# Optimization experiments

Measured on AMD Instinct MI355X. Metric: run time of the kernel, lower is better.

## Reference

```python
import jax, jax.numpy as jnp
import numpy as np

S, B, H = 4096, 1, 2048       # [seq, batch, hidden] layout (NeoX convention)
NP, HN = 16, H // 16          # heads, head dim
ROT = int(HN * 0.25)          # rotary_ndims = 32 (rotary_pct=0.25)
ROPE_BASE = 10000.0


def setup_inputs() -> dict:
    key = jax.random.key(0)
    k0, k1, k2 = jax.random.split(key, 3)
    hidden_states = jax.random.normal(k0, (S, B, H), jnp.float32) * 0.02
    # causal left-to-right mask: True = masked out (filled with -10000)
    attention_mask = jnp.triu(jnp.ones((1, 1, S, S), bool), k=1)
    w_qkv = jax.random.normal(k1, (3 * H, H), jnp.float32) * (1.0 / np.sqrt(H))
    w_dense = jax.random.normal(k2, (H, H), jnp.float32) * (1.0 / np.sqrt(H))
    b_dense = jnp.zeros((H,), jnp.float32)
    return {"hidden_states": hidden_states, "attention_mask": attention_mask,
            "w_qkv": w_qkv, "w_dense": w_dense, "b_dense": b_dense}


def _apply_rope(x, pos):
    # x: [s, b, np, ROT]; NeoX rotate_half convention
    inv_freq = 1.0 / (ROPE_BASE ** (jnp.arange(0, ROT, 2, dtype=jnp.float32) / ROT))
    freqs = pos[:, None] * inv_freq[None, :]              # [s, ROT/2]
    emb = jnp.concatenate([freqs, freqs], axis=-1)        # [s, ROT]
    cos = jnp.cos(emb)[:, None, None, :]
    sin = jnp.sin(emb)[:, None, None, :]
    x1, x2 = jnp.split(x, 2, axis=-1)
    rot = jnp.concatenate([-x2, x1], axis=-1)
    return x * cos + rot * sin


def reference(hidden_states, attention_mask, w_qkv, w_dense, b_dense):
    s, b, h = hidden_states.shape
    # fused QKV projection (no bias), reshape to [s, b, np, 3*hn], split
    qkv = (hidden_states @ w_qkv.T).reshape(s, b, NP, 3 * HN)
    q, k, v = jnp.split(qkv, 3, axis=-1)                  # each [s, b, np, hn]
    # partial rotary embedding on first ROT dims
    pos = jnp.arange(s, dtype=jnp.float32)
    q = jnp.concatenate([_apply_rope(q[..., :ROT], pos), q[..., ROT:]], axis=-1)
    k = jnp.concatenate([_apply_rope(k[..., :ROT], pos), k[..., ROT:]], axis=-1)
    # raw attention scores [b, np, s_q, s_k], scale 1/sqrt(hn)
    scores = jnp.einsum('sbhd,tbhd->bhst', q, k) / np.float32(np.sqrt(HN))
    # ltor mask: fill masked positions with -10000, softmax in fp32
    scores = jnp.where(attention_mask, jnp.float32(-10000.0), scores)
    probs = jax.nn.softmax(scores.astype(jnp.float32), axis=-1).astype(hidden_states.dtype)
    # context [s, b, np, hn] -> [s, b, h]
    ctx = jnp.einsum('bhst,tbhd->sbhd', probs, v).reshape(s, b, h)
    return ctx @ w_dense.T + b_dense
```

## Files before the change

### kernel.cpp

```cpp
#include <hip/hip_runtime.h>

#define S_LEN 4096
#define HID   2048
#define NHEAD 16
#define HDIM  128
#define QSCALE_L2E 0.12751664352f

typedef float  f32x4  __attribute__((ext_vector_type(4)));
typedef float  f32x16 __attribute__((ext_vector_type(16)));
typedef __bf16 bf16x8 __attribute__((ext_vector_type(8)));
typedef unsigned u32x4 __attribute__((ext_vector_type(4)));
typedef unsigned u32x2 __attribute__((ext_vector_type(2)));

#define MFMA16(a, b, c) __builtin_amdgcn_mfma_f32_16x16x32_bf16((a), (b), (c), 0, 0, 0)
#define MFMA32(a, b, c) __builtin_amdgcn_mfma_f32_32x32x16_bf16((a), (b), (c), 0, 0, 0)

__device__ __forceinline__ void gld16(const void* g, void* l) {
  __builtin_amdgcn_global_load_lds(
      (const __attribute__((address_space(1))) void*)(unsigned long long)(g),
      (__attribute__((address_space(3))) void*)(unsigned long long)(l),
      16, 0, 0);
}

__device__ __forceinline__ unsigned short f2bf(float f) {
  union { float f; unsigned u; } v; v.f = f;
  unsigned r = v.u + 0x7FFFu + ((v.u >> 16) & 1u);
  return (unsigned short)(r >> 16);
}
__device__ __forceinline__ float bf2f(unsigned short h) {
  union { unsigned u; float f; } v; v.u = ((unsigned)h) << 16;
  return v.f;
}
__device__ __forceinline__ unsigned cvtpk_bf16(float a, float b) {
  unsigned r;
  asm("v_cvt_pk_bf16_f32 %0, %1, %2" : "=v"(r) : "v"(a), "v"(b));
  return r;
}
__device__ __forceinline__ u32x2 pls(unsigned a, unsigned b) {
  return __builtin_amdgcn_permlane32_swap(a, b, false, false);
}
__device__ __forceinline__ float asf(unsigned u) { return __builtin_bit_cast(float, u); }
__device__ __forceinline__ unsigned asu(float f) { return __builtin_bit_cast(unsigned, f); }

__global__ __launch_bounds__(256) void cvt3_kernel(
    const float* __restrict__ s0, const float* __restrict__ s1,
    const float* __restrict__ s2, unsigned short* __restrict__ d0,
    unsigned short* __restrict__ d1, unsigned short* __restrict__ d2) {
  int i = (blockIdx.x * 256 + threadIdx.x) * 4;
  const float* src; unsigned short* dst;
  if (i < 8388608) { src = s0; dst = d0; }
  else if (i < 20971520) { src = s1 - 8388608; dst = d1 - 8388608; }
  else { src = s2 - 20971520; dst = d2 - 20971520; }
  const float4 v = *(const float4*)(src + i);
  ushort4 o;
  o.x = f2bf(v.x); o.y = f2bf(v.y); o.z = f2bf(v.z); o.w = f2bf(v.w);
  *(ushort4*)(dst + i) = o;
}

template <int EPI>
__global__ __launch_bounds__(512, 2) void gemm256_kernel(
    const unsigned short* __restrict__ A, const unsigned short* __restrict__ B,
    unsigned short* __restrict__ Qb, unsigned short* __restrict__ Kb,
    unsigned short* __restrict__ Vt,
    const float* __restrict__ bias, float* __restrict__ out) {
  __shared__ __align__(16) unsigned char sm[147456];
  constexpr int K = HID;
  constexpr int NT = K / 64;
  const int b = (int)blockIdx.x;
  const int bm = (b & 7) * 2 + ((b >> 3) & 1);
  const int bn = b >> 4;
  const int row0 = bm * 256, col0 = bn * 128;
  const int tid = threadIdx.x;
  const int wid = tid >> 6, lane = tid & 63;
  const int g = lane >> 4, r16 = lane & 15;
  const int wm = wid >> 1, wn = wid & 1;

  auto stageA = [&](int t, int bufo) {
    const int k0 = t * 64;
#pragma unroll
    for (int h = 0; h < 2; ++h)
#pragma unroll
      for (int cc = 0; cc < 2; ++cc) {
        const int chunk = cc * 512 + tid;
        const int r = chunk >> 3, c7 = chunk & 7;
        gld16(A + (row0 + h * 128 + r) * K + k0 + ((c7 ^ (r & 7)) << 3),
              sm + bufo + h * 16384 + chunk * 16);
      }
  };
  auto stageB = [&](int t, int bufo) {
    const int k0 = t * 64;
#pragma unroll
    for (int cc = 0; cc < 2; ++cc) {
      const int chunk = cc * 512 + tid;
      const int r = chunk >> 3, c7 = chunk & 7;
      gld16(B + (col0 + r) * K + k0 + ((c7 ^ (r & 7)) << 3),
            sm + bufo + 32768 + chunk * 16);
    }
  };

  f32x4 acc[4][4] = {};

  int aoff[4], boff[4];
#pragma unroll
  for (int m = 0; m < 4; ++m) {
    const int r = (wm & 1) * 64 + m * 16 + r16;
    aoff[m] = (wm >> 1) * 16384 + r * 128 + ((g * 16) ^ ((r & 7) << 4));
  }
#pragma unroll
  for (int n = 0; n < 4; ++n) {
    const int r = wn * 64 + n * 16 + r16;
    boff[n] = 32768 + r * 128 + ((g * 16) ^ ((r & 7) << 4));
  }

  stageA(0, 0); stageB(0, 0);
  stageA(1, 49152); stageB(1, 49152);
  asm volatile("s_waitcnt vmcnt(6)" ::: "memory");
  __builtin_amdgcn_s_barrier();
  __builtin_amdgcn_sched_barrier(0);

  int curo = 0, stgo = 98304;
  for (int t = 0; t < NT; ++t) {
    const bool st = (t + 2 < NT);
    bf16x8 af[4], bfv[4];
#pragma unroll
    for (int m = 0; m < 4; ++m) af[m] = *(const bf16x8*)(sm + curo + aoff[m]);
#pragma unroll
    for (int n = 0; n < 4; ++n) bfv[n] = *(const bf16x8*)(sm + curo + boff[n]);
    if (st) stageA(t + 2, stgo);
    __builtin_amdgcn_s_setprio(1);
#pragma unroll
    for (int m = 0; m < 4; ++m)
#pragma unroll
      for (int n = 0; n < 4; ++n) acc[m][n] = MFMA16(af[m], bfv[n], acc[m][n]);
    __builtin_amdgcn_s_setprio(0);
#pragma unroll
    for (int m = 0; m < 4; ++m) af[m] = *(const bf16x8*)(sm + curo + (aoff[m] ^ 64));
#pragma unroll
    for (int n = 0; n < 4; ++n) bfv[n] = *(const bf16x8*)(sm + curo + (boff[n] ^ 64));
    if (st) stageB(t + 2, stgo);
    __builtin_amdgcn_s_setprio(1);
#pragma unroll
    for (int m = 0; m < 4; ++m)
#pragma unroll
      for (int n = 0; n < 4; ++n) acc[m][n] = MFMA16(af[m], bfv[n], acc[m][n]);
    __builtin_amdgcn_s_setprio(0);
    if (st) asm volatile("s_waitcnt vmcnt(6)" ::: "memory");
    else    asm volatile("s_waitcnt vmcnt(0)" ::: "memory");
    __builtin_amdgcn_s_barrier();
    __builtin_amdgcn_sched_barrier(0);
    curo = (curo == 98304) ? 0 : curo + 49152;
    stgo = (stgo == 98304) ? 0 : stgo + 49152;
  }

  if constexpr (EPI == 0) {
    const int type = bn % 3, p = bn / 3;
    if (type <= 1) {
      unsigned short* Ob = (type == 0) ? Qb : Kb;
      const float qs = (type == 0) ? QSCALE_L2E : 1.0f;
      const float invf = exp2f(-(float)r16 * 0.8304820237218406f);
#pragma unroll
      for (int m = 0; m < 4; ++m) {
        const int s0 = row0 + wm * 64 + m * 16 + g * 4;
        if (wn == 0) {
#pragma unroll
          for (int r = 0; r < 4; ++r) {
            const float ang = (float)(s0 + r) * invf;
            const float c = cosf(ang), sn = sinf(ang);
            const float x = acc[m][0][r] * qs, y = acc[m][1][r] * qs;
            unsigned short* dst = Ob + (p * S_LEN + s0 + r) * HDIM;
            dst[r16]      = f2bf(x * c - y * sn);
            dst[16 + r16] = f2bf(y * c + x * sn);
          }
#pragma unroll
          for (int n = 2; n < 4; ++n)
#pragma unroll
            for (int r = 0; r < 4; ++r)
              Ob[(p * S_LEN + s0 + r) * HDIM + n * 16 + r16] = f2bf(acc[m][n][r] * qs);
        } else {
#pragma unroll
          for (int n = 0; n < 4; ++n)
#pragma unroll
            for (int r = 0; r < 4; ++r)
              Ob[(p * S_LEN + s0 + r) * HDIM + 64 + n * 16 + r16] = f2bf(acc[m][n][r] * qs);
        }
      }
    } else {
#pragma unroll
      for (int m = 0; m < 4; ++m) {
        const int s0 = row0 + wm * 64 + m * 16 + g * 4;
#pragma unroll
        for (int n = 0; n < 4; ++n) {
          const int d = wn * 64 + n * 16 + r16;
          ushort4 o;
          o.x = f2bf(acc[m][n][0]); o.y = f2bf(acc[m][n][1]);
          o.z = f2bf(acc[m][n][2]); o.w = f2bf(acc[m][n][3]);
          *(ushort4*)(Vt + (p * HDIM + d) * S_LEN + s0) = o;
        }
      }
    }
  } else {
#pragma unroll
    for (int m = 0; m < 4; ++m) {
      const int s0 = row0 + wm * 64 + m * 16 + g * 4;
#pragma unroll
      for (int n = 0; n < 4; ++n) {
        const int col = col0 + wn * 64 + n * 16 + r16;
        const float bv = bias[col];
#pragma unroll
        for (int r = 0; r < 4; ++r)
          out[(s0 + r) * HID + col] = acc[m][n][r] + bv;
      }
    }
  }
}

__global__ __launch_bounds__(512, 2) void attn_kernel(
    const unsigned short* __restrict__ Qb, const unsigned short* __restrict__ Kb,
    const unsigned short* __restrict__ Vt, unsigned short* __restrict__ Ctx) {
  __shared__ __align__(16) unsigned char sm[81920];
  const int b = (int)blockIdx.x;
  const int p = b & 15;
  const int qt = (b < 256) ? (b >> 4) : 47 - (b >> 4);
  const int tid = threadIdx.x, wid = tid >> 6, lane = tid & 63;
  const int g = wid >> 2, wv = wid & 3, gtid = tid & 255;
  const int l31 = lane & 31, hi = lane >> 5;
  const int xr = (l31 & 7) << 4;
  const int GB = g * 40960;

  const int q0w = qt * 128 + wv * 32;
  const int qg = q0w + l31;
  const int Th = 2 * (qt + 1);
  const int np = qt + 1;
  const int tg0 = g * Th;

  auto stageK = [&](int tg, int ko) {
    const unsigned short* kb = Kb + (p * S_LEN + tg * 32) * HDIM;
#pragma unroll
    for (int c = 0; c < 2; ++c) {
      const int chunk = c * 256 + gtid;
      const int j = chunk >> 4, cb = chunk & 15;
      gld16(kb + j * HDIM + ((cb ^ (j & 7)) << 3), sm + ko + chunk * 16);
    }
  };
  auto stageV = [&](int tg, int vo) {
    const unsigned short* vbase = Vt + p * HDIM * S_LEN + tg * 32;
#pragma unroll
    for (int c = 0; c < 2; ++c) {
      const int chunk = c * 256 + gtid;
      const int d = chunk >> 2, cb = chunk & 3;
      gld16(vbase + d * S_LEN + ((cb ^ (d & 3)) << 3), sm + vo + chunk * 16);
    }
  };

  bf16x8 qf[8];
  f32x16 acc[4] = {};
  float m_s = -1e30f, l_s = 0.f;

  auto qk = [&](f32x16& s, const unsigned char* kl) {
    __builtin_amdgcn_s_setprio(1);
#pragma unroll
    for (int dd = 0; dd < 8; ++dd) {
      bf16x8 k0 = *(const bf16x8*)(kl + l31 * 256 + (((dd * 2 + hi) << 4) ^ xr));
      s = MFMA32(k0, qf[dd], s);
    }
    __builtin_amdgcn_s_setprio(0);
  };

  auto smpv = [&](f32x16& s, int tg, int vo) {
    const unsigned char* vl = sm + vo;
    if (tg * 32 + 31 > q0w) {
#pragma unroll
      for (int r = 0; r < 16; ++r) {
        const int kv0 = tg * 32 + ((r & 3) + 8 * (r >> 2)) + 4 * hi;
        if (kv0 > qg) s[r] = -1e30f;
      }
    }
    float mx[8];
#pragma unroll
    for (int r = 0; r < 8; ++r) mx[r] = fmaxf(s[r], s[r + 8]);
#pragma unroll
    for (int r = 0; r < 4; ++r) mx[r] = fmaxf(mx[r], mx[r + 4]);
    mx[0] = fmaxf(fmaxf(mx[0], mx[2]), fmaxf(mx[1], mx[3]));
    float pm;
    {
      u32x2 e = pls(asu(mx[0]), asu(mx[0]));
      pm = fmaxf(asf(e.x), asf(e.y));
    }
    if (__any(pm > m_s + 11.5f)) {
      const float mn = fmaxf(m_s, pm);
      const float scl = exp2f(m_s - mn);
#pragma unroll
      for (int d32 = 0; d32 < 4; ++d32)
#pragma unroll
        for (int r = 0; r < 16; ++r) acc[d32][r] *= scl;
      l_s *= scl;
      m_s = mn;
    }
#pragma unroll
    for (int r = 0; r < 16; ++r) s[r] = exp2f(s[r] - m_s);
    bf16x8 pf[2];
#define PACKB(B, SV, base)                                                        \
    {                                                                             \
      unsigned X0 = cvtpk_bf16(SV[base + 0], SV[base + 1]);                       \
      unsigned X1 = cvtpk_bf16(SV[base + 2], SV[base + 3]);                       \
      unsigned Y0 = cvtpk_bf16(SV[base + 4], SV[base + 5]);                       \
      unsigned Y1 = cvtpk_bf16(SV[base + 6], SV[base + 7]);                       \
      u32x2 e0 = pls(X0, Y0);                                                     \
      u32x2 e1 = pls(X1, Y1);                                                     \
      u32x4 pw;                                                                   \
      pw.x = e0.x; pw.y = e1.x; pw.z = e0.y; pw.w = e1.y;                         \
      pf[B] = __builtin_bit_cast(bf16x8, pw);                                     \
    }
    PACKB(0, s, 0)
    PACKB(1, s, 8)
#undef PACKB
    __builtin_amdgcn_s_setprio(1);
#pragma unroll
    for (int d32 = 0; d32 < 4; ++d32) {
      const int d = d32 * 32 + l31;
#pragma unroll
      for (int bb = 0; bb < 2; ++bb) {
        bf16x8 vf = *(const bf16x8*)(vl + d * 64 + ((((bb * 2 + hi) << 4)) ^ ((l31 & 3) << 4)));
        acc[d32] = MFMA32(vf, pf[bb], acc[d32]);
      }
    }
    __builtin_amdgcn_s_setprio(0);
    float s_[8];
#pragma unroll
    for (int r = 0; r < 8; ++r) s_[r] = s[r] + s[r + 8];
#pragma unroll
    for (int r = 0; r < 4; ++r) s_[r] += s_[r + 4];
    const float rs = (s_[0] + s_[1]) + (s_[2] + s_[3]);
    u32x2 e = pls(asu(rs), asu(rs));
    l_s += asf(e.x) + asf(e.y);
  };

  {
    const unsigned short* qp_ = Qb + (p * S_LEN + qg) * HDIM + hi * 8;
#pragma unroll
    for (int dd = 0; dd < 8; ++dd) qf[dd] = *(const bf16x8*)(qp_ + dd * 16);
  }
  stageK(tg0, GB);
  stageV(tg0, GB + 16384);
  stageK(tg0 + 1, GB + 8192);
  stageV(tg0 + 1, GB + 24576);
  int vcur = GB + 16384, vnext = GB + 24576, vstage = GB + 32768;
  __syncthreads();
  f32x16 sA = {};
  qk(sA, sm + GB);
  __syncthreads();

  for (int tt = 0; tt < np; ++tt) {
    const bool more = (tt + 1 < np);
    const int t = tg0 + 2 * tt;
    f32x16 sB = {};
    qk(sB, sm + GB + 8192);
    if (more) { stageK(t + 2, GB); stageV(t + 2, vstage); }
    smpv(sA, t, vcur);
    { int tmp = vcur; vcur = vnext; vnext = vstage; vstage = tmp; }
    __syncthreads();
    if (more) {
      sA = {};
      qk(sA, sm + GB);
      stageK(t + 3, GB + 8192);
      stageV(t + 3, vstage);
    }
    smpv(sB, t + 1, vcur);
    { int tmp = vcur; vcur = vnext; vnext = vstage; vstage = tmp; }
    __syncthreads();
  }

  if (g == 1) {
    const int base = wv * 16384;
#pragma unroll
    for (int d32 = 0; d32 < 4; ++d32)
#pragma unroll
      for (int k = 0; k < 4; ++k) {
        float4 v4;
        v4.x = acc[d32][k * 4 + 0]; v4.y = acc[d32][k * 4 + 1];
        v4.z = acc[d32][k * 4 + 2]; v4.w = acc[d32][k * 4 + 3];
        *(float4*)(sm + base + d32 * 4096 + k * 1024 + lane * 16) = v4;
      }
    if (hi == 0)
      *(float2*)(sm + 65536 + (wv * 32 + l31) * 8) = make_float2(m_s, l_s);
  }
  __syncthreads();
  if (g == 0) {
    const float2 ml1 = *(const float2*)(sm + 65536 + (wv * 32 + l31) * 8);
    const float mm = fmaxf(m_s, ml1.x);
    const float w0 = exp2f(m_s - mm), w1 = exp2f(ml1.x - mm);
    const float linv = 1.0f / (l_s * w0 + ml1.y * w1);
    unsigned short* cbase = Ctx + qg * HID + p * HDIM;
#pragma unroll
    for (int d32 = 0; d32 < 4; ++d32)
#pragma unroll
      for (int k = 0; k < 4; ++k) {
        const float4 o1 = *(const float4*)(sm + wv * 16384 + d32 * 4096 + k * 1024 + lane * 16);
        const float ov[4] = {o1.x, o1.y, o1.z, o1.w};
#pragma unroll
        for (int j = 0; j < 4; ++j) {
          const int d = d32 * 32 + j + 8 * k + 4 * hi;
          cbase[d] = f2bf((acc[d32][k * 4 + j] * w0 + ov[j] * w1) * linv);
        }
      }
  }
}

extern "C" void kernel_launch(void* const* d_in, const int* in_sizes, int n_in,
                              void* d_out, int out_size, void* d_ws, size_t ws_size,
                              hipStream_t stream) {
  (void)in_sizes; (void)n_in; (void)out_size; (void)ws_size;
  const float* hidden = (const float*)d_in[0];
  const float* wqkv   = (const float*)d_in[2];
  const float* wdense = (const float*)d_in[3];
  const float* bdense = (const float*)d_in[4];
  float* out = (float*)d_out;

  char* ws = (char*)d_ws;
  unsigned short* hiddenB = (unsigned short*)(ws);
  unsigned short* wqkvB   = (unsigned short*)(ws + 16777216);
  unsigned short* wdenseB = (unsigned short*)(ws + 41943040);
  unsigned short* Qb      = (unsigned short*)(ws + 50331648);
  unsigned short* Kb      = (unsigned short*)(ws + 67108864);
  unsigned short* Vt      = (unsigned short*)(ws + 83886080);
  unsigned short* ctxB    = (unsigned short*)(ws + 100663296);

  cvt3_kernel<<<24576, 256, 0, stream>>>(hidden, wqkv, wdense, hiddenB, wqkvB, wdenseB);
  gemm256_kernel<0><<<768, 512, 0, stream>>>(hiddenB, wqkvB, Qb, Kb, Vt, nullptr, nullptr);
  attn_kernel<<<512, 512, 0, stream>>>(Qb, Kb, Vt, ctxB);
  gemm256_kernel<1><<<256, 512, 0, stream>>>(ctxB, wdenseB, nullptr, nullptr, nullptr, bdense, out);
}
```

Baseline: 282.2 us.

## Shrink GEMM K-tile to 32 for occupancy and split dense GEMM into 128x128 tiles

The templated GEMM is split into two kernels. The QKV GEMM now stages a K-step of 32 instead of 64, which cuts LDS use from 144KB to 72KB and raises the occupancy hint to 4 blocks per CU. The dense output GEMM now uses 128x128 tiles with 256 threads over 512 blocks, up from 256 blocks, so more of the CUs get work. The trade-off is twice as many loop iterations and barriers per K, and less data reuse per block in the dense GEMM.

```diff
diff --git a/kernel.cpp b/kernel.cpp
--- a/kernel.cpp
+++ b/kernel.cpp
@@ -57,15 +57,13 @@
   *(ushort4*)(dst + i) = o;
 }
 
-template <int EPI>
-__global__ __launch_bounds__(512, 2) void gemm256_kernel(
+__global__ __launch_bounds__(512, 4) void gemm_qkv_kernel(
     const unsigned short* __restrict__ A, const unsigned short* __restrict__ B,
     unsigned short* __restrict__ Qb, unsigned short* __restrict__ Kb,
-    unsigned short* __restrict__ Vt,
-    const float* __restrict__ bias, float* __restrict__ out) {
-  __shared__ __align__(16) unsigned char sm[147456];
+    unsigned short* __restrict__ Vt) {
+  __shared__ __align__(16) unsigned char sm[73728];
   constexpr int K = HID;
-  constexpr int NT = K / 64;
+  constexpr int NT = K / 32;
   const int b = (int)blockIdx.x;
   const int bm = (b & 7) * 2 + ((b >> 3) & 1);
   const int bn = b >> 4;
@@ -76,49 +74,40 @@
   const int wm = wid >> 1, wn = wid & 1;
 
   auto stageA = [&](int t, int bufo) {
-    const int k0 = t * 64;
-#pragma unroll
-    for (int h = 0; h < 2; ++h)
-#pragma unroll
-      for (int cc = 0; cc < 2; ++cc) {
-        const int chunk = cc * 512 + tid;
-        const int r = chunk >> 3, c7 = chunk & 7;
-        gld16(A + (row0 + h * 128 + r) * K + k0 + ((c7 ^ (r & 7)) << 3),
-              sm + bufo + h * 16384 + chunk * 16);
-      }
-  };
-  auto stageB = [&](int t, int bufo) {
-    const int k0 = t * 64;
+    const int k0 = t * 32;
 #pragma unroll
     for (int cc = 0; cc < 2; ++cc) {
       const int chunk = cc * 512 + tid;
-      const int r = chunk >> 3, c7 = chunk & 7;
-      gld16(B + (col0 + r) * K + k0 + ((c7 ^ (r & 7)) << 3),
-            sm + bufo + 32768 + chunk * 16);
-    }
+      const int r = chunk >> 2, c3 = chunk & 3;
+      gld16(A + (row0 + r) * K + k0 + ((c3 ^ (r & 3)) << 3), sm + bufo + chunk * 16);
+    }
+  };
+  auto stageB = [&](int t, int bufo) {
+    const int k0 = t * 32;
+    const int r = tid >> 2, c3 = tid & 3;
+    gld16(B + (col0 + r) * K + k0 + ((c3 ^ (r & 3)) << 3), sm + bufo + 16384 + tid * 16);
   };
 
   f32x4 acc[4][4] = {};
-
   int aoff[4], boff[4];
 #pragma unroll
   for (int m = 0; m < 4; ++m) {
-    const int r = (wm & 1) * 64 + m * 16 + r16;
-    aoff[m] = (wm >> 1) * 16384 + r * 128 + ((g * 16) ^ ((r & 7) << 4));
+    const int r = wm * 64 + m * 16 + r16;
+    aoff[m] = r * 64 + ((g * 16) ^ ((r & 3) << 4));
   }
 #pragma unroll
   for (int n = 0; n < 4; ++n) {
     const int r = wn * 64 + n * 16 + r16;
-    boff[n] = 32768 + r * 128 + ((g * 16) ^ ((r & 7) << 4));
+    boff[n] = 16384 + r * 64 + ((g * 16) ^ ((r & 3) << 4));
   }
 
   stageA(0, 0); stageB(0, 0);
-  stageA(1, 49152); stageB(1, 49152);
-  asm volatile("s_waitcnt vmcnt(6)" ::: "memory");
+  stageA(1, 24576); stageB(1, 24576);
+  asm volatile("s_waitcnt vmcnt(3)" ::: "memory");
   __builtin_amdgcn_s_barrier();
   __builtin_amdgcn_sched_barrier(0);
 
-  int curo = 0, stgo = 98304;
+  int curo = 0, stgo = 49152;
   for (int t = 0; t < NT; ++t) {
     const bool st = (t + 2 < NT);
     bf16x8 af[4], bfv[4];
@@ -126,90 +115,154 @@
     for (int m = 0; m < 4; ++m) af[m] = *(const bf16x8*)(sm + curo + aoff[m]);
 #pragma unroll
     for (int n = 0; n < 4; ++n) bfv[n] = *(const bf16x8*)(sm + curo + boff[n]);
-    if (st) stageA(t + 2, stgo);
+    if (st) { stageA(t + 2, stgo); stageB(t + 2, stgo); }
     __builtin_amdgcn_s_setprio(1);
 #pragma unroll
     for (int m = 0; m < 4; ++m)
 #pragma unroll
       for (int n = 0; n < 4; ++n) acc[m][n] = MFMA16(af[m], bfv[n], acc[m][n]);
     __builtin_amdgcn_s_setprio(0);
-#pragma unroll
-    for (int m = 0; m < 4; ++m) af[m] = *(const bf16x8*)(sm + curo + (aoff[m] ^ 64));
-#pragma unroll
-    for (int n = 0; n < 4; ++n) bfv[n] = *(const bf16x8*)(sm + curo + (boff[n] ^ 64));
-    if (st) stageB(t + 2, stgo);
-    __builtin_amdgcn_s_setprio(1);
-#pragma unroll
-    for (int m = 0; m < 4; ++m)
-#pragma unroll
-      for (int n = 0; n < 4; ++n) acc[m][n] = MFMA16(af[m], bfv[n], acc[m][n]);
-    __builtin_amdgcn_s_setprio(0);
-    if (st) asm volatile("s_waitcnt vmcnt(6)" ::: "memory");
+    if (st) asm volatile("s_waitcnt vmcnt(3)" ::: "memory");
     else    asm volatile("s_waitcnt vmcnt(0)" ::: "memory");
     __builtin_amdgcn_s_barrier();
     __builtin_amdgcn_sched_barrier(0);
-    curo = (curo == 98304) ? 0 : curo + 49152;
-    stgo = (stgo == 98304) ? 0 : stgo + 49152;
-  }
-
-  if constexpr (EPI == 0) {
-    const int type = bn % 3, p = bn / 3;
-    if (type <= 1) {
-      unsigned short* Ob = (type == 0) ? Qb : Kb;
-      const float qs = (type == 0) ? QSCALE_L2E : 1.0f;
-      const float invf = exp2f(-(float)r16 * 0.8304820237218406f);
-#pragma unroll
-      for (int m = 0; m < 4; ++m) {
-        const int s0 = row0 + wm * 64 + m * 16 + g * 4;
-        if (wn == 0) {
-#pragma unroll
-          for (int r = 0; r < 4; ++r) {
-            const float ang = (float)(s0 + r) * invf;
-            const float c = cosf(ang), sn = sinf(ang);
-            const float x = acc[m][0][r] * qs, y = acc[m][1][r] * qs;
-            unsigned short* dst = Ob + (p * S_LEN + s0 + r) * HDIM;
-            dst[r16]      = f2bf(x * c - y * sn);
-            dst[16 + r16] = f2bf(y * c + x * sn);
-          }
-#pragma unroll
-          for (int n = 2; n < 4; ++n)
-#pragma unroll
-            for (int r = 0; r < 4; ++r)
-              Ob[(p * S_LEN + s0 + r) * HDIM + n * 16 + r16] = f2bf(acc[m][n][r] * qs);
-        } else {
-#pragma unroll
-          for (int n = 0; n < 4; ++n)
-#pragma unroll
-            for (int r = 0; r < 4; ++r)
-              Ob[(p * S_LEN + s0 + r) * HDIM + 64 + n * 16 + r16] = f2bf(acc[m][n][r] * qs);
-        }
-      }
-    } else {
-#pragma unroll
-      for (int m = 0; m < 4; ++m) {
-        const int s0 = row0 + wm * 64 + m * 16 + g * 4;
-#pragma unroll
-        for (int n = 0; n < 4; ++n) {
-          const int d = wn * 64 + n * 16 + r16;
-          ushort4 o;
-          o.x = f2bf(acc[m][n][0]); o.y = f2bf(acc[m][n][1]);
-          o.z = f2bf(acc[m][n][2]); o.w = f2bf(acc[m][n][3]);
-          *(ushort4*)(Vt + (p * HDIM + d) * S_LEN + s0) = o;
-        }
-      }
-    }
-  } else {
+    curo = (curo == 49152) ? 0 : curo + 24576;
+    stgo = (stgo == 49152) ? 0 : stgo + 24576;
+  }
+
+  const int type = bn % 3, p = bn / 3;
+  if (type <= 1) {
+    unsigned short* Ob = (type == 0) ? Qb : Kb;
+    const float qs = (type == 0) ? QSCALE_L2E : 1.0f;
+    const float invf = exp2f(-(float)r16 * 0.8304820237218406f);
 #pragma unroll
     for (int m = 0; m < 4; ++m) {
       const int s0 = row0 + wm * 64 + m * 16 + g * 4;
+      if (wn == 0) {
+#pragma unroll
+        for (int r = 0; r < 4; ++r) {
+          const float ang = (float)(s0 + r) * invf;
+          const float c = cosf(ang), sn = sinf(ang);
+          const float x = acc[m][0][r] * qs, y = acc[m][1][r] * qs;
+          unsigned short* dst = Ob + (p * S_LEN + s0 + r) * HDIM;
+          dst[r16]      = f2bf(x * c - y * sn);
+          dst[16 + r16] = f2bf(y * c + x * sn);
+        }
+#pragma unroll
+        for (int n = 2; n < 4; ++n)
+#pragma unroll
+          for (int r = 0; r < 4; ++r)
+            Ob[(p * S_LEN + s0 + r) * HDIM + n * 16 + r16] = f2bf(acc[m][n][r] * qs);
+      } else {
+#pragma unroll
+        for (int n = 0; n < 4; ++n)
+#pragma unroll
+          for (int r = 0; r < 4; ++r)
+            Ob[(p * S_LEN + s0 + r) * HDIM + 64 + n * 16 + r16] = f2bf(acc[m][n][r] * qs);
+      }
+    }
+  } else {
+#pragma unroll
+    for (int m = 0; m < 4; ++m) {
+      const int s0 = row0 + wm * 64 + m * 16 + g * 4;
 #pragma unroll
       for (int n = 0; n < 4; ++n) {
-        const int col = col0 + wn * 64 + n * 16 + r16;
-        const float bv = bias[col];
-#pragma unroll
-        for (int r = 0; r < 4; ++r)
-          out[(s0 + r) * HID + col] = acc[m][n][r] + bv;
-      }
+        const int d = wn * 64 + n * 16 + r16;
+        ushort4 o;
+        o.x = f2bf(acc[m][n][0]); o.y = f2bf(acc[m][n][1]);
+        o.z = f2bf(acc[m][n][2]); o.w = f2bf(acc[m][n][3]);
+        *(ushort4*)(Vt + (p * HDIM + d) * S_LEN + s0) = o;
+      }
+    }
+  }
+}
+
+__global__ __launch_bounds__(256, 4) void gemm_dense_kernel(
+    const unsigned short* __restrict__ A, const unsigned short* __restrict__ B,
+    const float* __restrict__ bias, float* __restrict__ out) {
+  __shared__ __align__(16) unsigned char sm[49152];
+  constexpr int K = HID;
+  constexpr int NT = K / 32;
+  const int b = (int)blockIdx.x;
+  const int bm = (b & 7) * 4 + ((b >> 3) & 3);
+  const int bn = b >> 5;
+  const int row0 = bm * 128, col0 = bn * 128;
+  const int tid = threadIdx.x;
+  const int wid = tid >> 6, lane = tid & 63;
+  const int g = lane >> 4, r16 = lane & 15;
+  const int wm = wid >> 1, wn = wid & 1;
+
+  auto stageA = [&](int t, int bufo) {
+    const int k0 = t * 32;
+#pragma unroll
+    for (int cc = 0; cc < 2; ++cc) {
+      const int chunk = cc * 256 + tid;
+      const int r = chunk >> 2, c3 = chunk & 3;
+      gld16(A + (row0 + r) * K + k0 + ((c3 ^ (r & 3)) << 3), sm + bufo + chunk * 16);
+    }
+  };
+  auto stageB = [&](int t, int bufo) {
+    const int k0 = t * 32;
+#pragma unroll
+    for (int cc = 0; cc < 2; ++cc) {
+      const int chunk = cc * 256 + tid;
+      const int r = chunk >> 2, c3 = chunk & 3;
+      gld16(B + (col0 + r) * K + k0 + ((c3 ^ (r & 3)) << 3), sm + bufo + 8192 + chunk * 16);
+    }
+  };
+
+  f32x4 acc[4][4] = {};
+  int aoff[4], boff[4];
+#pragma unroll
+  for (int m = 0; m < 4; ++m) {
+    const int r = wm * 64 + m * 16 + r16;
+    aoff[m] = r * 64 + ((g * 16) ^ ((r & 3) << 4));
+  }
+#pragma unroll
+  for (int n = 0; n < 4; ++n) {
+    const int r = wn * 64 + n * 16 + r16;
+    boff[n] = 8192 + r * 64 + ((g * 16) ^ ((r & 3) << 4));
+  }
+
+  stageA(0, 0); stageB(0, 0);
+  stageA(1, 16384); stageB(1, 16384);
+  asm volatile("s_waitcnt vmcnt(4)" ::: "memory");
+  __builtin_amdgcn_s_barrier();
+  __builtin_amdgcn_sched_barrier(0);
+
+  int curo = 0, stgo = 32768;
+  for (int t = 0; t < NT; ++t) {
+    const bool st = (t + 2 < NT);
+    bf16x8 af[4], bfv[4];
+#pragma unroll
+    for (int m = 0; m < 4; ++m) af[m] = *(const bf16x8*)(sm + curo + aoff[m]);
+#pragma unroll
+    for (int n = 0; n < 4; ++n) bfv[n] = *(const bf16x8*)(sm + curo + boff[n]);
+    if (st) { stageA(t + 2, stgo); stageB(t + 2, stgo); }
+    __builtin_amdgcn_s_setprio(1);
+#pragma unroll
+    for (int m = 0; m < 4; ++m)
+#pragma unroll
+      for (int n = 0; n < 4; ++n) acc[m][n] = MFMA16(af[m], bfv[n], acc[m][n]);
+    __builtin_amdgcn_s_setprio(0);
+    if (st) asm volatile("s_waitcnt vmcnt(4)" ::: "memory");
+    else    asm volatile("s_waitcnt vmcnt(0)" ::: "memory");
+    __builtin_amdgcn_s_barrier();
+    __builtin_amdgcn_sched_barrier(0);
+    curo = (curo == 32768) ? 0 : curo + 16384;
+    stgo = (stgo == 32768) ? 0 : stgo + 16384;
+  }
+
+#pragma unroll
+  for (int m = 0; m < 4; ++m) {
+    const int s0 = row0 + wm * 64 + m * 16 + g * 4;
+#pragma unroll
+    for (int n = 0; n < 4; ++n) {
+      const int col = col0 + wn * 64 + n * 16 + r16;
+      const float bv = bias[col];
+#pragma unroll
+      for (int r = 0; r < 4; ++r)
+        out[(s0 + r) * HID + col] = acc[m][n][r] + bv;
     }
   }
 }
@@ -426,7 +479,7 @@
   unsigned short* ctxB    = (unsigned short*)(ws + 100663296);
 
   cvt3_kernel<<<24576, 256, 0, stream>>>(hidden, wqkv, wdense, hiddenB, wqkvB, wdenseB);
-  gemm256_kernel<0><<<768, 512, 0, stream>>>(hiddenB, wqkvB, Qb, Kb, Vt, nullptr, nullptr);
+  gemm_qkv_kernel<<<768, 512, 0, stream>>>(hiddenB, wqkvB, Qb, Kb, Vt);
   attn_kernel<<<512, 512, 0, stream>>>(Qb, Kb, Vt, ctxB);
-  gemm256_kernel<1><<<256, 512, 0, stream>>>(ctxB, wdenseB, nullptr, nullptr, nullptr, bdense, out);
-}
+  gemm_dense_kernel<<<512, 256, 0, stream>>>(ctxB, wdenseB, bdense, out);
+}
```

Result: no change. 282.7 us (+0.2%).
